# Kernel tuning notes

Hardware: AMD Instinct MI355X
Metric: run time of the kernel (lower is better)

The kernel has to match this reference:

```python
import jax, jax.numpy as jnp
import numpy as np
from jax import lax

B, CR, CS = 2, 256, 512
HR = WR = 64
HS = WS = 32
D_INNER, D_STATE, DT_RANK, D_CONV = 512, 16, 16, 3
EPS = 1e-5


def setup_inputs() -> dict:
    key = jax.random.key(0)
    ks = jax.random.split(key, 16)
    s = 0.02
    return {
        "resnet_feat": jax.random.normal(ks[0], (B, CR, HR, WR), jnp.float32),
        "scp_feat": jax.random.normal(ks[1], (B, CS, HS, WS), jnp.float32),
        "scp_proj_w": jax.random.normal(ks[2], (CR, CS), jnp.float32) * s,
        "scp_bn_g": jnp.ones((CR,), jnp.float32),
        "scp_bn_b": jnp.zeros((CR,), jnp.float32),
        "scp_bn_m": jax.random.normal(ks[3], (CR,), jnp.float32) * 0.1,
        "scp_bn_v": jax.random.uniform(ks[4], (CR,), jnp.float32, minval=0.5, maxval=1.5),
        "res_bn_g": jnp.ones((CR,), jnp.float32),
        "res_bn_b": jnp.zeros((CR,), jnp.float32),
        "res_bn_m": jax.random.normal(ks[5], (CR,), jnp.float32) * 0.1,
        "res_bn_v": jax.random.uniform(ks[6], (CR,), jnp.float32, minval=0.5, maxval=1.5),
        "ln_g": jnp.ones((CR,), jnp.float32),
        "ln_b": jnp.zeros((CR,), jnp.float32),
        "in_proj_w": jax.random.normal(ks[7], (2 * D_INNER, CR), jnp.float32) * s,
        "conv_w": jax.random.normal(ks[8], (D_INNER, 1, D_CONV), jnp.float32) * s,
        "conv_b": jnp.zeros((D_INNER,), jnp.float32),
        "x_proj_w": jax.random.normal(ks[9], (DT_RANK + 2 * D_STATE, D_INNER), jnp.float32) * s,
        "dt_proj_w": jax.random.normal(ks[10], (D_INNER, DT_RANK), jnp.float32) * s,
        "dt_proj_b": jnp.full((D_INNER,), -4.6, jnp.float32),  # softplus -> dt ~ 0.01
        "A_log": jnp.log(jnp.broadcast_to(jnp.arange(1, D_STATE + 1, dtype=jnp.float32), (D_INNER, D_STATE))),
        "D": jnp.ones((D_INNER,), jnp.float32),
        "out_proj_w": jax.random.normal(ks[11], (CR, D_INNER), jnp.float32) * s,
    }


def _bn(x, g, b, m, v):
    # eval-mode BatchNorm2d with running stats, NCHW
    inv = g / jnp.sqrt(v + EPS)
    return x * inv[None, :, None, None] + (b - m * inv)[None, :, None, None]


def reference(resnet_feat, scp_feat, scp_proj_w, scp_bn_g, scp_bn_b, scp_bn_m, scp_bn_v,
              res_bn_g, res_bn_b, res_bn_m, res_bn_v, ln_g, ln_b, in_proj_w, conv_w, conv_b,
              x_proj_w, dt_proj_w, dt_proj_b, A_log, D, out_proj_w):
    # --- fusion prelude ---
    rn = _bn(resnet_feat, res_bn_g, res_bn_b, res_bn_m, res_bn_v)
    sp = jnp.einsum('bchw,oc->bohw', scp_feat, scp_proj_w)        # 1x1 conv, no bias
    sp = _bn(sp, scp_bn_g, scp_bn_b, scp_bn_m, scp_bn_v)
    sp = jax.image.resize(sp, (B, CR, HR, WR), method='bilinear')  # align_corners=False semantics
    fused = rn + sp                                               # (B, CR, HR, WR)

    # --- Mamba2DBlock ---
    L = HR * WR
    x_seq = fused.transpose(0, 2, 3, 1).reshape(B, L, CR)
    mu = x_seq.mean(-1, keepdims=True)
    var = x_seq.var(-1, keepdims=True)
    xn = (x_seq - mu) / jnp.sqrt(var + EPS) * ln_g + ln_b         # LayerNorm

    xz = xn @ in_proj_w.T                                         # (B, L, 2*d_inner)
    xm, z = jnp.split(xz, 2, axis=-1)

    # causal depthwise conv1d over sequence
    xc = xm.transpose(0, 2, 1)                                    # (B, d_inner, L)
    xc = jnp.pad(xc, ((0, 0), (0, 0), (D_CONV - 1, 0)))
    xc = lax.conv_general_dilated(xc, conv_w, (1,), 'VALID',
                                  dimension_numbers=('NCH', 'OIH', 'NCH'),
                                  feature_group_count=D_INNER) + conv_b[None, :, None]
    u = jax.nn.silu(xc.transpose(0, 2, 1))                        # (B, L, d_inner)

    x_dbl = u @ x_proj_w.T                                        # (B, L, dt_rank + 2*d_state)
    dt_in, Bc, Cc = jnp.split(x_dbl, [DT_RANK, DT_RANK + D_STATE], axis=-1)
    dt = jax.nn.softplus(dt_in @ dt_proj_w.T + dt_proj_b)         # (B, L, d_inner)

    A = -jnp.exp(A_log)                                           # (d_inner, d_state)
    dA = jnp.exp(dt[..., None] * A)                               # (B, L, d_inner, d_state)
    dBu = dt[..., None] * Bc[:, :, None, :] * u[..., None]        # (B, L, d_inner, d_state)

    def comb(c1, c2):
        a1, b1 = c1
        a2, b2 = c2
        return a1 * a2, a2 * b1 + b2

    _, h = lax.associative_scan(comb, (dA, dBu), axis=1)          # h: (B, L, d_inner, d_state)
    y = jnp.einsum('blds,bls->bld', h, Cc) + u * D
    y = y * jax.nn.silu(z)
    out_seq = y @ out_proj_w.T                                    # (B, L, CR)
    out = out_seq.reshape(B, HR, WR, CR).transpose(0, 3, 1, 2)
    return fused + out
```

## Files before the change

### kernel.cpp

```cpp
#include <hip/hip_runtime.h>
#include <hip/hip_bf16.h>
#include <math.h>

typedef unsigned short u16;
typedef __attribute__((ext_vector_type(8))) short short8;
typedef __attribute__((ext_vector_type(4))) float f32x4;
typedef __attribute__((ext_vector_type(4))) unsigned short u16x4;

#define DEVINL static __device__ __forceinline__

DEVINL float b2f(u16 x) {
    union { unsigned u; float f; } v; v.u = ((unsigned)x) << 16; return v.f;
}
DEVINL u16 f2b(float f) {
    union { unsigned u; float f; } v; v.f = f;
    unsigned u = v.u;
    return (u16)((u + 0x7fffu + ((u >> 16) & 1u)) >> 16);
}
DEVINL float silu(float x) { return x * __fdividef(1.f, 1.f + __expf(-x)); }
DEVINL float ld_any(bool f32, const void* p, size_t i) {
    return f32 ? ((const float*)p)[i] : b2f(((const u16*)p)[i]);
}
template<bool F32> DEVINL float LDs(const void* p, size_t i) {
    if constexpr (F32) return ((const float*)p)[i];
    else               return b2f(((const u16*)p)[i]);
}

DEVINL bool detect_f32(const u16* __restrict__ raw) {
    int cnt = 0;
#pragma unroll
    for (int i = 0; i < 64; ++i) {
        float v = b2f(raw[i * 2]);
        if (!(fabsf(v) <= 1e3f)) cnt++;
    }
    return cnt > 0;
}

#define O_INW  0
#define O_XPW  262144
#define O_OPW  286720
#define O_SPW  417792
#define O_CW   548864
#define O_CB   550400
#define O_DTW  550912
#define O_ALOG 559104
#define O_DTB  567296
#define O_DW   567808
#define O_SG   568320
#define O_SB   568576
#define O_SM   568832
#define O_SV   569088
#define O_RG   569344
#define O_RB   569600
#define O_RM   569856
#define O_RV   570112
#define O_LG   570368
#define O_LB   570624
#define N_CVT  570880
#define O_FLAG 570880


DEVINL void tr_tile(bool f32, const void* src, u16* dst, int R, int C,
                    int c0, int r0, int b, int tid)
{
    __shared__ u16 t[64][66];
    int lane = tid & 63, grp = tid >> 6;
#pragma unroll
    for (int j = 0; j < 16; ++j) {
        int rl = j * 4 + grp;
        t[rl][lane] = f2b(ld_any(f32, src, ((size_t)b * R + r0 + rl) * C + c0 + lane));
    }
    __syncthreads();
#pragma unroll
    for (int j = 0; j < 16; ++j) {
        int cl = j * 4 + grp;
        dst[((size_t)b * C + c0 + cl) * R + r0 + lane] = t[lane][cl];
    }
}

__global__ __launch_bounds__(256) void k_prep(
    const void* inw, const void* xpw, const void* opw, const void* spw,
    const void* cw, const void* cb, const void* dtw, const void* alog,
    const void* dtb, const void* Dw,
    const void* sg, const void* sb, const void* sm, const void* sv,
    const void* rg, const void* rb, const void* rm, const void* rv,
    const void* lg, const void* lb,
    const void* scp, const void* resnet,
    u16* __restrict__ w16, u16* __restrict__ scpT, u16* __restrict__ resnetT)
{
    bool f32 = detect_f32((const u16*)resnet);
    int bid = blockIdx.x, tid = threadIdx.x;
    if (bid < 2230) {
        int i = bid * 256 + tid;
        const void* src; int off = i;
        if      (i < O_XPW)  { src = inw; }
        else if (i < O_OPW)  { src = xpw;  off = i - O_XPW; }
        else if (i < O_SPW)  { src = opw;  off = i - O_OPW; }
        else if (i < O_CW)   { src = spw;  off = i - O_SPW; }
        else if (i < O_CB)   { src = cw;   off = i - O_CW; }
        else if (i < O_DTW)  { src = cb;   off = i - O_CB; }
        else if (i < O_ALOG) { src = dtw;  off = i - O_DTW; }
        else if (i < O_DTB)  { src = alog; off = i - O_ALOG; }
        else if (i < O_DW)   { src = dtb;  off = i - O_DTB; }
        else if (i < O_SG)   { src = Dw;   off = i - O_DW; }
        else if (i < O_SB)   { src = sg;   off = i - O_SG; }
        else if (i < O_SM)   { src = sb;   off = i - O_SB; }
        else if (i < O_SV)   { src = sm;   off = i - O_SM; }
        else if (i < O_RG)   { src = sv;   off = i - O_SV; }
        else if (i < O_RB)   { src = rg;   off = i - O_RG; }
        else if (i < O_RM)   { src = rb;   off = i - O_RB; }
        else if (i < O_RV)   { src = rm;   off = i - O_RM; }
        else if (i < O_LG)   { src = rv;   off = i - O_RV; }
        else if (i < O_LB)   { src = lg;   off = i - O_LG; }
        else                 { src = lb;   off = i - O_LB; }
        w16[i] = f2b(ld_any(f32, src, off));
    } else if (bid < 2230 + 256) {
        int t = bid - 2230;
        tr_tile(f32, scp, scpT, 512, 1024, (t & 15) * 64, ((t >> 4) & 7) * 64, t >> 7, tid);
    } else if (bid < 2998) {
        int t = bid - 2486;
        tr_tile(f32, resnet, resnetT, 256, 4096, (t & 63) * 64, ((t >> 6) & 3) * 64, t >> 8, tid);
    } else {
        __shared__ int oksh;
        if (tid == 0) oksh = 1;
        __syncthreads();
        bool ok = true;
        for (int i = tid; i < 512 * 16; i += 256) {
            int s = i & 15;
            float av = -__expf(ld_any(f32, alog, i));
            if (fabsf(av + (float)(s + 1)) > 0.03f * (float)(s + 1)) ok = false;
        }
        if (!ok) atomicAnd(&oksh, 0);
        __syncthreads();
        if (tid == 0) w16[O_FLAG] = (u16)oksh;
    }
}

__global__ __launch_bounds__(256) void k_scpmm(
    const u16* __restrict__ scpT, const u16* __restrict__ w16,
    u16* __restrict__ sp16)
{
    const int N = 256, K = 512;
    int tid = threadIdx.x, lane = tid & 63, wid = tid >> 6;
    int ln = lane & 15, q = lane >> 4;
    int m0 = blockIdx.x * 64 + (wid & 1) * 32;
    int n0 = blockIdx.y * 64 + (wid >> 1) * 32;
    f32x4 acc00 = {0.f,0.f,0.f,0.f}, acc01 = acc00, acc10 = acc00, acc11 = acc00;
    const u16* Ap0 = scpT + (size_t)(m0 + ln) * K + q * 8;
    const u16* Ap1 = Ap0 + (size_t)16 * K;
    const u16* Wp = w16 + O_SPW;
#pragma unroll 4
    for (int k0 = 0; k0 < K; k0 += 32) {
        int kk = k0 + q * 8;
        short8 a0 = *reinterpret_cast<const short8*>(Ap0 + k0);
        short8 a1 = *reinterpret_cast<const short8*>(Ap1 + k0);
        short8 b0 = *reinterpret_cast<const short8*>(Wp + (size_t)(n0 + ln) * K + kk);
        short8 b1 = *reinterpret_cast<const short8*>(Wp + (size_t)(n0 + ln + 16) * K + kk);
        acc00 = __builtin_amdgcn_mfma_f32_16x16x32_bf16(a0, b0, acc00, 0, 0, 0);
        acc01 = __builtin_amdgcn_mfma_f32_16x16x32_bf16(a0, b1, acc01, 0, 0, 0);
        acc10 = __builtin_amdgcn_mfma_f32_16x16x32_bf16(a1, b0, acc10, 0, 0, 0);
        acc11 = __builtin_amdgcn_mfma_f32_16x16x32_bf16(a1, b1, acc11, 0, 0, 0);
    }
    int r0 = m0 + q * 4, c0 = n0 + ln;
    float inv0 = b2f(w16[O_SG + c0]) * rsqrtf(b2f(w16[O_SV + c0]) + 1e-5f);
    float sh0  = b2f(w16[O_SB + c0]) - b2f(w16[O_SM + c0]) * inv0;
    float inv1 = b2f(w16[O_SG + c0 + 16]) * rsqrtf(b2f(w16[O_SV + c0 + 16]) + 1e-5f);
    float sh1  = b2f(w16[O_SB + c0 + 16]) - b2f(w16[O_SM + c0 + 16]) * inv1;
#pragma unroll
    for (int r = 0; r < 4; ++r) {
        sp16[(size_t)(r0 + r) * N + c0]           = f2b(acc00[r] * inv0 + sh0);
        sp16[(size_t)(r0 + r) * N + c0 + 16]      = f2b(acc01[r] * inv1 + sh1);
        sp16[(size_t)(r0 + 16 + r) * N + c0]      = f2b(acc10[r] * inv0 + sh0);
        sp16[(size_t)(r0 + 16 + r) * N + c0 + 16] = f2b(acc11[r] * inv1 + sh1);
    }
}

__global__ __launch_bounds__(256) void k_ln(
    const u16* __restrict__ resnetT, const u16* __restrict__ w16,
    const u16* __restrict__ sp16, u16* __restrict__ xn)
{
    __shared__ float red[8];
    int c = threadIdx.x, b = blockIdx.y;
    float inv = b2f(w16[O_RG + c]) * rsqrtf(b2f(w16[O_RV + c]) + 1e-5f);
    float sh  = b2f(w16[O_RB + c]) - b2f(w16[O_RM + c]) * inv;
    float lgv = b2f(w16[O_LG + c]), lbv = b2f(w16[O_LB + c]);
    const u16* spc = sp16 + (size_t)b * 1024 * 256 + c;
    for (int j = 0; j < 8; ++j) {
        int l = blockIdx.x * 8 + j;
        int h = l >> 6, w = l & 63;
        float rr = b2f(resnetT[((size_t)b * 4096 + l) * 256 + c]);
        float rn = rr * inv + sh;
        float xh = 0.5f * h - 0.25f; int jh = (int)floorf(xh); float fh = xh - jh;
        float xw = 0.5f * w - 0.25f; int jw = (int)floorf(xw); float fw = xw - jw;
        int h0 = jh < 0 ? 0 : jh, h1 = jh + 1 > 31 ? 31 : jh + 1;
        int w0 = jw < 0 ? 0 : jw, w1 = jw + 1 > 31 ? 31 : jw + 1;
        float v00 = b2f(spc[(size_t)(h0 * 32 + w0) * 256]), v01 = b2f(spc[(size_t)(h0 * 32 + w1) * 256]);
        float v10 = b2f(spc[(size_t)(h1 * 32 + w0) * 256]), v11 = b2f(spc[(size_t)(h1 * 32 + w1) * 256]);
        float sp = (1.f - fh) * ((1.f - fw) * v00 + fw * v01)
                 + fh * ((1.f - fw) * v10 + fw * v11);
        float fv = rn + sp;

        float s = fv, s2 = fv * fv;
#pragma unroll
        for (int off = 1; off < 64; off <<= 1) {
            s  += __shfl_xor(s, off);
            s2 += __shfl_xor(s2, off);
        }
        int wv = c >> 6;
        if ((c & 63) == 0) { red[wv] = s; red[4 + wv] = s2; }
        __syncthreads();
        float S  = red[0] + red[1] + red[2] + red[3];
        float S2 = red[4] + red[5] + red[6] + red[7];
        __syncthreads();
        float mu   = S * (1.f / 256.f);
        float var  = S2 * (1.f / 256.f) - mu * mu;
        float rstd = rsqrtf(var + 1e-5f);
        xn[((size_t)b * 4096 + l) * 256 + c] = f2b((fv - mu) * rstd * lgv + lbv);
    }
}

__global__ __launch_bounds__(256) void k_gemm_in(
    const u16* __restrict__ A, const u16* __restrict__ w16, u16* __restrict__ Out)
{
    const int N = 1024, K = 256;
    int tid = threadIdx.x, lane = tid & 63, wid = tid >> 6;
    int ln = lane & 15, q = lane >> 4;
    int m0 = blockIdx.x * 128 + (wid & 1) * 64;
    int n0 = blockIdx.y * 128 + (wid >> 1) * 64;
    f32x4 acc[4][4];
#pragma unroll
    for (int i = 0; i < 4; ++i)
#pragma unroll
        for (int j = 0; j < 4; ++j) acc[i][j] = {0.f,0.f,0.f,0.f};
    const u16* Ap = A + (size_t)(m0 + ln) * K + q * 8;
    const u16* Bp = w16 + O_INW + (size_t)(n0 + ln) * K + q * 8;
#pragma unroll
    for (int k0 = 0; k0 < K; k0 += 32) {
        short8 a[4], bb[4];
#pragma unroll
        for (int i = 0; i < 4; ++i)
            a[i] = *reinterpret_cast<const short8*>(Ap + (size_t)(16 * i) * K + k0);
#pragma unroll
        for (int j = 0; j < 4; ++j)
            bb[j] = *reinterpret_cast<const short8*>(Bp + (size_t)(16 * j) * K + k0);
#pragma unroll
        for (int i = 0; i < 4; ++i)
#pragma unroll
            for (int j = 0; j < 4; ++j)
                acc[i][j] = __builtin_amdgcn_mfma_f32_16x16x32_bf16(a[i], bb[j], acc[i][j], 0, 0, 0);
    }
    int r0 = m0 + q * 4, c0 = n0 + ln;
#pragma unroll
    for (int i = 0; i < 4; ++i)
#pragma unroll
        for (int j = 0; j < 4; ++j)
#pragma unroll
            for (int r = 0; r < 4; ++r)
                Out[(size_t)(r0 + 16 * i + r) * N + c0 + 16 * j] = f2b(acc[i][j][r]);
}

DEVINL short8 u_frag(const u16* __restrict__ xz, const u16* __restrict__ w16,
                     int row, int kk0)
{
    int l = row & 4095;
    const u16* p = xz + (size_t)row * 1024 + kk0;
    short8 zz = {0,0,0,0,0,0,0,0};
    short8 x0 = *reinterpret_cast<const short8*>(p);
    short8 x1 = (l >= 1) ? *reinterpret_cast<const short8*>(p - 1024) : zz;
    short8 x2 = (l >= 2) ? *reinterpret_cast<const short8*>(p - 2048) : zz;
    short8 r;
#pragma unroll
    for (int j = 0; j < 8; ++j) {
        int d = kk0 + j;
        float acc = b2f(w16[O_CB + d])
                  + b2f((u16)x2[j]) * b2f(w16[O_CW + d * 3])
                  + b2f((u16)x1[j]) * b2f(w16[O_CW + d * 3 + 1])
                  + b2f((u16)x0[j]) * b2f(w16[O_CW + d * 3 + 2]);
        r[j] = (short)f2b(silu(acc));
    }
    return r;
}

__global__ __launch_bounds__(256) void k_xproj(
    const u16* __restrict__ xz, const u16* __restrict__ w16, float* __restrict__ xdf)
{
    __shared__ float xred[4][64][12];
    int tid = threadIdx.x, lane = tid & 63, wid = tid >> 6;
    int ln = lane & 15, q = lane >> 4;
    int m0 = blockIdx.x * 16;
    const u16* Wp = w16 + O_XPW;
    f32x4 acc[3];
#pragma unroll
    for (int j = 0; j < 3; ++j) acc[j] = {0.f,0.f,0.f,0.f};
    int kb = wid * 128;
    for (int k0 = kb; k0 < kb + 128; k0 += 32) {
        int kk0 = k0 + q * 8;
        short8 a0 = u_frag(xz, w16, m0 + ln, kk0);
#pragma unroll
        for (int j = 0; j < 3; ++j) {
            short8 bj = *reinterpret_cast<const short8*>(Wp + (size_t)(16 * j + ln) * 512 + kk0);
            acc[j] = __builtin_amdgcn_mfma_f32_16x16x32_bf16(a0, bj, acc[j], 0, 0, 0);
        }
    }
#pragma unroll
    for (int j = 0; j < 3; ++j)
#pragma unroll
        for (int r = 0; r < 4; ++r) xred[wid][lane][j * 4 + r] = acc[j][r];
    __syncthreads();
    if (wid == 0) {
#pragma unroll
        for (int j = 0; j < 3; ++j)
#pragma unroll
            for (int r = 0; r < 4; ++r) {
                float v = xred[0][lane][j * 4 + r] + xred[1][lane][j * 4 + r]
                        + xred[2][lane][j * 4 + r] + xred[3][lane][j * 4 + r];
                xdf[(size_t)(m0 + q * 4 + r) * 48 + 16 * j + ln] = v;
            }
    }
}

#define SCAN_PRELUDE()                                                        \
    const float* xr = xr0 + (size_t)il * 48;                                  \
    float x0 = b2f(xz[xbase + (size_t)il * 1024]);                            \
    float uv = silu(cbv + cw0 * x2 + cw1 * x1 + cw2 * x0);                    \
    float pa = 0.f, pb = 0.f, pc = 0.f, pq = 0.f;                             \
    _Pragma("unroll")                                                         \
    for (int j = 0; j < 4; ++j) {                                             \
        pa += xr[j]      * wdt[j];      pb += xr[4 + j]  * wdt[4 + j];        \
        pc += xr[8 + j]  * wdt[8 + j];  pq += xr[12 + j] * wdt[12 + j];       \
    }                                                                         \
    float accd = bias + ((pa + pb) + (pc + pq));                              \
    float dtv = accd > 15.f ? accd : __logf(1.f + __expf(accd));              \
    float du = dtv * uv;

__global__ __launch_bounds__(512) void k_scan1(
    const u16* __restrict__ xz, const float* __restrict__ xdf,
    const u16* __restrict__ w16, unsigned* __restrict__ cAH,
    int NC, int CL)
{
    int d = threadIdx.x, ck = blockIdx.x, b = blockIdx.y;
    float wdt[16];
#pragma unroll
    for (int j = 0; j < 16; ++j) wdt[j] = b2f(w16[O_DTW + d * 16 + j]);
    float bias = b2f(w16[O_DTB + d]);
    float cw0 = b2f(w16[O_CW + d * 3]), cw1 = b2f(w16[O_CW + d * 3 + 1]),
          cw2 = b2f(w16[O_CW + d * 3 + 2]), cbv = b2f(w16[O_CB + d]);
    int l0 = ck * CL;
    size_t xbase = ((size_t)b * 4096 + l0) * 1024 + d;
    float x2 = (l0 >= 2) ? b2f(xz[xbase - 2048]) : 0.f;
    float x1 = (l0 >= 1) ? b2f(xz[xbase - 1024]) : 0.f;
    const float* xr0 = xdf + ((size_t)b * 4096 + l0) * 48;
    size_t obase = (((size_t)b * NC + ck) * 16) * 512 + d;
    float h[16];
#pragma unroll
    for (int s = 0; s < 16; ++s) h[s] = 0.f;

    if (w16[O_FLAG]) {
        float sdt = 0.f;
#pragma unroll 2
        for (int il = 0; il < CL; ++il) {
            SCAN_PRELUDE();
            sdt += dtv;
            float e1 = __expf(-dtv);
            float e2 = e1 * e1, e3 = e2 * e1, e4 = e2 * e2;
            float e8 = e4 * e4, e12 = e8 * e4;
            float inn[4] = {e1, e2, e3, e4};
            float bas[4] = {1.f, e4, e8, e12};
#pragma unroll
            for (int s = 0; s < 16; ++s)
                h[s] = (bas[s >> 2] * inn[s & 3]) * h[s] + du * xr[16 + s];
            x2 = x1; x1 = x0;
        }
        float E1 = __expf(-sdt);
        float E2 = E1 * E1, E3 = E2 * E1, E4 = E2 * E2;
        float E8 = E4 * E4, E12 = E8 * E4;
        float iN[4] = {E1, E2, E3, E4};
        float bA[4] = {1.f, E4, E8, E12};
#pragma unroll
        for (int s = 0; s < 16; ++s)
            cAH[obase + (size_t)s * 512] =
                (unsigned)f2b(bA[s >> 2] * iN[s & 3]) | ((unsigned)f2b(h[s]) << 16);
    } else {
        float a[16], ap[16];
#pragma unroll
        for (int s = 0; s < 16; ++s) {
            a[s] = -__expf(b2f(w16[O_ALOG + d * 16 + s]));
            ap[s] = 1.f;
        }
        for (int il = 0; il < CL; ++il) {
            SCAN_PRELUDE();
#pragma unroll
            for (int s = 0; s < 16; ++s) {
                float dA = __expf(dtv * a[s]);
                h[s] = dA * h[s] + du * xr[16 + s];
                ap[s] *= dA;
            }
            x2 = x1; x1 = x0;
        }
#pragma unroll
        for (int s = 0; s < 16; ++s)
            cAH[obase + (size_t)s * 512] =
                (unsigned)f2b(ap[s]) | ((unsigned)f2b(h[s]) << 16);
    }
}

__global__ __launch_bounds__(128) void k_scan2(
    const unsigned* __restrict__ cAH, u16* __restrict__ hIn, int NC)
{
    int d = blockIdx.y * 128 + threadIdx.x, s = blockIdx.x, b = blockIdx.z;
    float h = 0.f;
#pragma unroll 8
    for (int ck = 0; ck < NC; ++ck) {
        size_t idx = (((size_t)b * NC + ck) * 16 + s) * 512 + d;
        unsigned v = cAH[idx];
        float aP = b2f((u16)(v & 0xffffu));
        float hE = b2f((u16)(v >> 16));
        hIn[idx] = f2b(h);
        h = aP * h + hE;
    }
}

__global__ __launch_bounds__(512) void k_scan3(
    const u16* __restrict__ xz, const float* __restrict__ xdf,
    const u16* __restrict__ w16, const u16* __restrict__ hIn,
    u16* __restrict__ y, int NC, int CL)
{
    int d = threadIdx.x, ck = blockIdx.x, b = blockIdx.y;
    float wdt[16];
#pragma unroll
    for (int j = 0; j < 16; ++j) wdt[j] = b2f(w16[O_DTW + d * 16 + j]);
    float bias = b2f(w16[O_DTB + d]);
    float Dv = b2f(w16[O_DW + d]);
    float cw0 = b2f(w16[O_CW + d * 3]), cw1 = b2f(w16[O_CW + d * 3 + 1]),
          cw2 = b2f(w16[O_CW + d * 3 + 2]), cbv = b2f(w16[O_CB + d]);
    int l0 = ck * CL;
    size_t xbase = ((size_t)b * 4096 + l0) * 1024 + d;
    float x2 = (l0 >= 2) ? b2f(xz[xbase - 2048]) : 0.f;
    float x1 = (l0 >= 1) ? b2f(xz[xbase - 1024]) : 0.f;
    const float* xr0 = xdf + ((size_t)b * 4096 + l0) * 48;
    size_t obase = (((size_t)b * NC + ck) * 16) * 512 + d;
    float h[16];
#pragma unroll
    for (int s = 0; s < 16; ++s) h[s] = b2f(hIn[obase + (size_t)s * 512]);

    if (w16[O_FLAG]) {
#pragma unroll 2
        for (int il = 0; il < CL; ++il) {
            SCAN_PRELUDE();
            float e1 = __expf(-dtv);
            float e2 = e1 * e1, e3 = e2 * e1, e4 = e2 * e2;
            float e8 = e4 * e4, e12 = e8 * e4;
            float inn[4] = {e1, e2, e3, e4};
            float bas[4] = {1.f, e4, e8, e12};
            float yv = 0.f;
#pragma unroll
            for (int s = 0; s < 16; ++s) {
                h[s] = (bas[s >> 2] * inn[s & 3]) * h[s] + du * xr[16 + s];
                yv += h[s] * xr[32 + s];
            }
            size_t row = (size_t)b * 4096 + l0 + il;
            yv += uv * Dv;
            float zv = b2f(xz[row * 1024 + 512 + d]);
            yv *= silu(zv);
            y[row * 512 + d] = f2b(yv);
            x2 = x1; x1 = x0;
        }
    } else {
        float a[16];
#pragma unroll
        for (int s = 0; s < 16; ++s)
            a[s] = -__expf(b2f(w16[O_ALOG + d * 16 + s]));
        for (int il = 0; il < CL; ++il) {
            SCAN_PRELUDE();
            float yv = 0.f;
#pragma unroll
            for (int s = 0; s < 16; ++s) {
                float dA = __expf(dtv * a[s]);
                h[s] = dA * h[s] + du * xr[16 + s];
                yv += h[s] * xr[32 + s];
            }
            size_t row = (size_t)b * 4096 + l0 + il;
            yv += uv * Dv;
            float zv = b2f(xz[row * 1024 + 512 + d]);
            yv *= silu(zv);
            y[row * 512 + d] = f2b(yv);
            x2 = x1; x1 = x0;
        }
    }
}

template<bool F32> DEVINL void out_body(
    const u16* Y, const u16* w16, const void* resnet,
    const u16* sp16, void* outp)
{
    const int K = 512;
    int tid = threadIdx.x, lane = tid & 63, wid = tid >> 6;
    int ln = lane & 15, q = lane >> 4;
    int m0 = blockIdx.x * 64 + (wid & 1) * 32;
    int n0 = blockIdx.y * 128 + (wid >> 1) * 64;
    f32x4 acc[2][4];
#pragma unroll
    for (int i = 0; i < 2; ++i)
#pragma unroll
        for (int j = 0; j < 4; ++j) acc[i][j] = {0.f,0.f,0.f,0.f};
    const u16* Ap0 = w16 + O_OPW + (size_t)(m0 + ln) * K + q * 8;
    const u16* Ap1 = Ap0 + (size_t)16 * K;
    const u16* Bp  = Y + (size_t)(n0 + ln) * K + q * 8;
#pragma unroll 2
    for (int k0 = 0; k0 < K; k0 += 32) {
        short8 a0 = *reinterpret_cast<const short8*>(Ap0 + k0);
        short8 a1 = *reinterpret_cast<const short8*>(Ap1 + k0);
#pragma unroll
        for (int j = 0; j < 4; ++j) {
            short8 bj = *reinterpret_cast<const short8*>(Bp + (size_t)(16 * j) * K + k0);
            acc[0][j] = __builtin_amdgcn_mfma_f32_16x16x32_bf16(a0, bj, acc[0][j], 0, 0, 0);
            acc[1][j] = __builtin_amdgcn_mfma_f32_16x16x32_bf16(a1, bj, acc[1][j], 0, 0, 0);
        }
    }
    int r0 = m0 + q * 4;
    int nb = n0 + ln;
    float inv8[2][4], sh8[2][4];
#pragma unroll
    for (int im = 0; im < 2; ++im)
#pragma unroll
        for (int r = 0; r < 4; ++r) {
            int c = r0 + 16 * im + r;
            float inv = b2f(w16[O_RG + c]) * rsqrtf(b2f(w16[O_RV + c]) + 1e-5f);
            inv8[im][r] = inv;
            sh8[im][r]  = b2f(w16[O_RB + c]) - b2f(w16[O_RM + c]) * inv;
        }
#pragma unroll
    for (int jn = 0; jn < 4; ++jn) {
        int n = nb + 16 * jn;
        int b = n >> 12, l = n & 4095;
        int hh = l >> 6, w = l & 63;
        float xh = 0.5f * hh - 0.25f; int jh = (int)floorf(xh); float fh = xh - jh;
        float xw = 0.5f * w - 0.25f;  int jw = (int)floorf(xw); float fw = xw - jw;
        int h0 = jh < 0 ? 0 : jh, h1 = jh + 1 > 31 ? 31 : jh + 1;
        int w0 = jw < 0 ? 0 : jw, w1 = jw + 1 > 31 ? 31 : jw + 1;
        float w00 = (1.f - fh) * (1.f - fw), w01 = (1.f - fh) * fw;
        float w10 = fh * (1.f - fw),         w11 = fh * fw;
        const u16* spb = sp16 + (size_t)b * 1024 * 256;
#pragma unroll
        for (int im = 0; im < 2; ++im) {
            int cb = r0 + 16 * im;
            u16x4 s00 = *reinterpret_cast<const u16x4*>(spb + (size_t)(h0 * 32 + w0) * 256 + cb);
            u16x4 s01 = *reinterpret_cast<const u16x4*>(spb + (size_t)(h0 * 32 + w1) * 256 + cb);
            u16x4 s10 = *reinterpret_cast<const u16x4*>(spb + (size_t)(h1 * 32 + w0) * 256 + cb);
            u16x4 s11 = *reinterpret_cast<const u16x4*>(spb + (size_t)(h1 * 32 + w1) * 256 + cb);
#pragma unroll
            for (int r = 0; r < 4; ++r) {
                int c = cb + r;
                float rr = LDs<F32>(resnet, ((size_t)b * 256 + c) * 4096 + l);
                float sp = w00 * b2f(s00[r]) + w01 * b2f(s01[r])
                         + w10 * b2f(s10[r]) + w11 * b2f(s11[r]);
                float val = acc[im][jn][r] + rr * inv8[im][r] + sh8[im][r] + sp;
                size_t oi = ((size_t)b * 256 + c) * 4096 + l;
                if constexpr (F32) ((float*)outp)[oi] = val;
                else               ((u16*)outp)[oi]  = f2b(val);
            }
        }
    }
}
__global__ __launch_bounds__(256) void k_out(
    const u16* Y, const u16* w16, const void* resnet,
    const u16* sp16, void* outp)
{
    if (detect_f32((const u16*)resnet)) out_body<true>(Y, w16, resnet, sp16, outp);
    else                                out_body<false>(Y, w16, resnet, sp16, outp);
}

extern "C" void kernel_launch(void* const* d_in, const int* in_sizes, int n_in,
                              void* d_out, int out_size, void* d_ws, size_t ws_size,
                              hipStream_t stream)
{
    const void* resnet = d_in[0];
    const void* scp    = d_in[1];
    const void* spw    = d_in[2];
    const void* sg     = d_in[3];
    const void* sb     = d_in[4];
    const void* sm     = d_in[5];
    const void* sv     = d_in[6];
    const void* rg     = d_in[7];
    const void* rb     = d_in[8];
    const void* rm     = d_in[9];
    const void* rv     = d_in[10];
    const void* lg     = d_in[11];
    const void* lb     = d_in[12];
    const void* inw    = d_in[13];
    const void* cw     = d_in[14];
    const void* cb     = d_in[15];
    const void* xpw    = d_in[16];
    const void* dtw    = d_in[17];
    const void* dtb    = d_in[18];
    const void* alog   = d_in[19];
    const void* Dw     = d_in[20];
    const void* opw    = d_in[21];

    char*  ws      = (char*)d_ws;
    u16*   w16     = (u16*)(ws + 4096);
    u16*   sp16    = (u16*)(ws + 2097152);
    u16*   scpT    = (u16*)(ws + 4194304);
    u16*   resnetT = (u16*)(ws + 8388608);
    u16*   xn      = (u16*)(ws + 12582912);
    u16*   xz      = (u16*)(ws + 16777216);
    float* xdf     = (float*)(ws + 33554432);
    u16*   y       = (u16*)(ws + 35651584);
    const size_t tail0 = 44040192;

    int NC = 16;
    for (int cand = 256; cand >= 16; cand >>= 1) {
        if (tail0 + (size_t)cand * 98304 <= ws_size) { NC = cand; break; }
    }
    int CL = 4096 / NC;
    unsigned* cAH = (unsigned*)(ws + tail0);
    u16*      hIn = (u16*)(ws + tail0 + (size_t)NC * 65536);

    k_prep<<<dim3(2999), 256, 0, stream>>>(
        inw, xpw, opw, spw, cw, cb, dtw, alog, dtb, Dw,
        sg, sb, sm, sv, rg, rb, rm, rv, lg, lb,
        scp, resnet, w16, scpT, resnetT);
    k_scpmm<<<dim3(32, 4), 256, 0, stream>>>(scpT, w16, sp16);
    k_ln<<<dim3(512, 2), 256, 0, stream>>>(resnetT, w16, sp16, xn);
    k_gemm_in<<<dim3(64, 8), 256, 0, stream>>>(xn, w16, xz);
    k_xproj<<<dim3(512), 256, 0, stream>>>(xz, w16, xdf);
    k_scan1<<<dim3(NC, 2), 512, 0, stream>>>(xz, xdf, w16, cAH, NC, CL);
    k_scan2<<<dim3(16, 4, 2), 128, 0, stream>>>(cAH, hIn, NC);
    k_scan3<<<dim3(NC, 2), 512, 0, stream>>>(xz, xdf, w16, hIn, y, NC, CL);
    k_out<<<dim3(4, 64), 256, 0, stream>>>(y, w16, resnet, sp16, d_out);
}
```

Measured before the change: 240.9 us.

## Fuse x_proj GEMM into scan1 and stage per-chunk x_dbl rows in LDS

When the chunk length is 16 (NC=256), scan1 now computes the x_proj projection for its own 16 rows with MFMA. Each of its 8 waves handles a 64-wide K slice, and the partial sums are reduced through shared memory. The result is written to xdf for scan3 and also kept in LDS for the scan loop, so the separate k_xproj launch is skipped. scan3 also stages its 16x48 x_dbl tile in LDS instead of reading global memory in the inner loop. The change removes a kernel launch and repeated global reads, at the cost of extra shared memory and reduction work at the start of scan1.

Result: slower. 270.1 us (+12.1%).

```diff
diff --git a/kernel.cpp b/kernel.cpp
--- a/kernel.cpp
+++ b/kernel.cpp
@@ -334,22 +334,70 @@
     float du = dtv * uv;
 
 __global__ __launch_bounds__(512) void k_scan1(
-    const u16* __restrict__ xz, const float* __restrict__ xdf,
+    const u16* __restrict__ xz, float* __restrict__ xdf,
     const u16* __restrict__ w16, unsigned* __restrict__ cAH,
-    int NC, int CL)
-{
-    int d = threadIdx.x, ck = blockIdx.x, b = blockIdx.y;
+    int NC, int CL, int fuseXp)
+{
+    __shared__ float xred[8][64][12];
+    __shared__ float xds[16][48];
+    int tid = threadIdx.x, d = tid, ck = blockIdx.x, b = blockIdx.y;
+    int l0 = ck * CL;
+
+    if (fuseXp) {
+        int lane = tid & 63, wid = tid >> 6;
+        int ln = lane & 15, q = lane >> 4;
+        int m0 = b * 4096 + l0;
+        const u16* Wp = w16 + O_XPW;
+        f32x4 acc[3];
+#pragma unroll
+        for (int j = 0; j < 3; ++j) acc[j] = {0.f,0.f,0.f,0.f};
+        int kb = wid * 64;
+        for (int k0 = kb; k0 < kb + 64; k0 += 32) {
+            int kk0 = k0 + q * 8;
+            short8 a0 = u_frag(xz, w16, m0 + ln, kk0);
+#pragma unroll
+            for (int j = 0; j < 3; ++j) {
+                short8 bj = *reinterpret_cast<const short8*>(Wp + (size_t)(16 * j + ln) * 512 + kk0);
+                acc[j] = __builtin_amdgcn_mfma_f32_16x16x32_bf16(a0, bj, acc[j], 0, 0, 0);
+            }
+        }
+#pragma unroll
+        for (int j = 0; j < 3; ++j)
+#pragma unroll
+            for (int r = 0; r < 4; ++r) xred[wid][lane][j * 4 + r] = acc[j][r];
+        __syncthreads();
+        if (wid == 0) {
+#pragma unroll
+            for (int j = 0; j < 3; ++j)
+#pragma unroll
+                for (int r = 0; r < 4; ++r) {
+                    float v = 0.f;
+#pragma unroll
+                    for (int w8 = 0; w8 < 8; ++w8) v += xred[w8][lane][j * 4 + r];
+                    int rr = q * 4 + r, cc = 16 * j + ln;
+                    xds[rr][cc] = v;
+                    xdf[(size_t)(m0 + rr) * 48 + cc] = v;
+                }
+        }
+        __syncthreads();
+    } else if (CL == 16) {
+        for (int i = tid; i < 16 * 48; i += 512)
+            (&xds[0][0])[i] = xdf[((size_t)(b * 4096 + l0)) * 48 + i];
+        __syncthreads();
+    }
+
+    const float* xr0 = (CL == 16) ? &xds[0][0]
+                                  : xdf + ((size_t)b * 4096 + l0) * 48;
+
     float wdt[16];
 #pragma unroll
     for (int j = 0; j < 16; ++j) wdt[j] = b2f(w16[O_DTW + d * 16 + j]);
     float bias = b2f(w16[O_DTB + d]);
     float cw0 = b2f(w16[O_CW + d * 3]), cw1 = b2f(w16[O_CW + d * 3 + 1]),
           cw2 = b2f(w16[O_CW + d * 3 + 2]), cbv = b2f(w16[O_CB + d]);
-    int l0 = ck * CL;
     size_t xbase = ((size_t)b * 4096 + l0) * 1024 + d;
     float x2 = (l0 >= 2) ? b2f(xz[xbase - 2048]) : 0.f;
     float x1 = (l0 >= 1) ? b2f(xz[xbase - 1024]) : 0.f;
-    const float* xr0 = xdf + ((size_t)b * 4096 + l0) * 48;
     size_t obase = (((size_t)b * NC + ck) * 16) * 512 + d;
     float h[16];
 #pragma unroll
@@ -425,7 +473,17 @@
     const u16* __restrict__ w16, const u16* __restrict__ hIn,
     u16* __restrict__ y, int NC, int CL)
 {
-    int d = threadIdx.x, ck = blockIdx.x, b = blockIdx.y;
+    __shared__ float xds[16][48];
+    int tid = threadIdx.x, d = tid, ck = blockIdx.x, b = blockIdx.y;
+    int l0 = ck * CL;
+    if (CL == 16) {
+        for (int i = tid; i < 16 * 48; i += 512)
+            (&xds[0][0])[i] = xdf[((size_t)(b * 4096 + l0)) * 48 + i];
+        __syncthreads();
+    }
+    const float* xr0 = (CL == 16) ? &xds[0][0]
+                                  : xdf + ((size_t)b * 4096 + l0) * 48;
+
     float wdt[16];
 #pragma unroll
     for (int j = 0; j < 16; ++j) wdt[j] = b2f(w16[O_DTW + d * 16 + j]);
@@ -433,11 +491,9 @@
     float Dv = b2f(w16[O_DW + d]);
     float cw0 = b2f(w16[O_CW + d * 3]), cw1 = b2f(w16[O_CW + d * 3 + 1]),
           cw2 = b2f(w16[O_CW + d * 3 + 2]), cbv = b2f(w16[O_CB + d]);
-    int l0 = ck * CL;
     size_t xbase = ((size_t)b * 4096 + l0) * 1024 + d;
     float x2 = (l0 >= 2) ? b2f(xz[xbase - 2048]) : 0.f;
     float x1 = (l0 >= 1) ? b2f(xz[xbase - 1024]) : 0.f;
-    const float* xr0 = xdf + ((size_t)b * 4096 + l0) * 48;
     size_t obase = (((size_t)b * NC + ck) * 16) * 512 + d;
     float h[16];
 #pragma unroll
@@ -613,6 +669,7 @@
         if (tail0 + (size_t)cand * 98304 <= ws_size) { NC = cand; break; }
     }
     int CL = 4096 / NC;
+    int fuseXp = (CL == 16) ? 1 : 0;
     unsigned* cAH = (unsigned*)(ws + tail0);
     u16*      hIn = (u16*)(ws + tail0 + (size_t)NC * 65536);
 
@@ -623,8 +680,9 @@
     k_scpmm<<<dim3(32, 4), 256, 0, stream>>>(scpT, w16, sp16);
     k_ln<<<dim3(512, 2), 256, 0, stream>>>(resnetT, w16, sp16, xn);
     k_gemm_in<<<dim3(64, 8), 256, 0, stream>>>(xn, w16, xz);
-    k_xproj<<<dim3(512), 256, 0, stream>>>(xz, w16, xdf);
-    k_scan1<<<dim3(NC, 2), 512, 0, stream>>>(xz, xdf, w16, cAH, NC, CL);
+    if (!fuseXp)
+        k_xproj<<<dim3(512), 256, 0, stream>>>(xz, w16, xdf);
+    k_scan1<<<dim3(NC, 2), 512, 0, stream>>>(xz, xdf, w16, cAH, NC, CL, fuseXp);
     k_scan2<<<dim3(16, 4, 2), 128, 0, stream>>>(cAH, hIn, NC);
     k_scan3<<<dim3(NC, 2), 512, 0, stream>>>(xz, xdf, w16, hIn, y, NC, CL);
     k_out<<<dim3(4, 64), 256, 0, stream>>>(y, w16, resnet, sp16, d_out);
```
